# Performance work log

Measured on AMD Instinct MI355X. Metric: run time of the kernel, lower is better.

The kernel has to match this reference:

```python
import jax, jax.numpy as jnp
import numpy as np

EPS = 1e-5

def _layernorm(x, w, b):
    mu = jnp.mean(x, axis=-1, keepdims=True)
    var = jnp.mean(jnp.square(x - mu), axis=-1, keepdims=True)
    return (x - mu) * jax.lax.rsqrt(var + EPS) * w + b

def setup_inputs() -> dict:
    key = jax.random.key(0)
    ks = jax.random.split(key, 6)
    B, Np, Nc, D, P = 2, 512, 512, 128, 128
    p_embed = jax.random.normal(ks[0], (B, Np, D), dtype=jnp.float32)
    c_embed = jax.random.normal(ks[1], (B, Nc, D), dtype=jnp.float32)
    p_mask = jnp.ones((B, Np), dtype=bool)
    c_mask = jnp.ones((B, Nc), dtype=bool)
    ln_p_w = jnp.ones((D,), jnp.float32)
    ln_p_b = jnp.zeros((D,), jnp.float32)
    ln_c_w = jnp.ones((D,), jnp.float32)
    ln_c_b = jnp.zeros((D,), jnp.float32)
    W_out = jax.random.normal(ks[2], (P, D), dtype=jnp.float32) / np.sqrt(D)
    b_out = jax.random.normal(ks[3], (P,), dtype=jnp.float32) * 0.01
    return {"p_embed": p_embed, "c_embed": c_embed, "p_mask": p_mask,
            "c_mask": c_mask, "ln_p_w": ln_p_w, "ln_p_b": ln_p_b,
            "ln_c_w": ln_c_w, "ln_c_b": ln_c_b, "W_out": W_out, "b_out": b_out}

def reference(p_embed, c_embed, p_mask, c_mask, ln_p_w, ln_p_b, ln_c_w, ln_c_b, W_out, b_out):
    # inter_mask[b,i,j] = p_mask[b,i] & c_mask[b,j]
    inter_mask = p_mask[..., :, None] & c_mask[..., None, :]
    p = _layernorm(p_embed, ln_p_w, ln_p_b)  # [B,Np,D]
    c = _layernorm(c_embed, ln_c_w, ln_c_b)  # [B,Nc,D]
    # einsum '...ik,...jk->...ijk' followed by Linear(D->P), fused into one
    # contraction so the [B,Np,Nc,D] intermediate is never materialized:
    # out[b,i,j,h] = sum_k p[b,i,k]*c[b,j,k]*W_out[h,k] + b_out[h]
    inter = jnp.einsum('bik,bjk,hk->bijh', p, c, W_out) + b_out
    inter = inter * inter_mask[..., None].astype(inter.dtype)
    return inter, inter_mask
```

## Files before the change

### kernel.cpp

```cpp
#include <hip/hip_runtime.h>
#include <hip/hip_bf16.h>

#define BATCH 2
#define NP 512
#define NC 512
#define DD 128
#define PP 128

typedef __bf16 bf16_t;
typedef __bf16 bf16x8 __attribute__((ext_vector_type(8)));
typedef float f32x4 __attribute__((ext_vector_type(4)));

__global__ __launch_bounds__(64) void ln_kernel(const float* __restrict__ x,
                                                const float* __restrict__ w,
                                                const float* __restrict__ bsh,
                                                float* __restrict__ y) {
    int row = blockIdx.x;
    int t = threadIdx.x;
    const float* xr = x + (size_t)row * DD;
    float2 v = *(const float2*)&xr[2 * t];
    float s  = v.x + v.y;
    float sq = v.x * v.x + v.y * v.y;
    for (int o = 32; o; o >>= 1) {
        s  += __shfl_xor(s, o);
        sq += __shfl_xor(sq, o);
    }
    float mu  = s * (1.0f / 128.0f);
    float var = sq * (1.0f / 128.0f) - mu * mu;
    float rs  = rsqrtf(var + 1e-5f);
    float2 wv = *(const float2*)&w[2 * t];
    float2 bv = *(const float2*)&bsh[2 * t];
    float* yr = y + (size_t)row * DD;
    float2 o2;
    o2.x = (v.x - mu) * rs * wv.x + bv.x;
    o2.y = (v.y - mu) * rs * wv.y + bv.y;
    *(float2*)&yr[2 * t] = o2;
}

__global__ __launch_bounds__(256) void cvt_kernel(const float* __restrict__ W,
                                                  bf16_t* __restrict__ Wb) {
    int idx = blockIdx.x * 256 + threadIdx.x;
    Wb[idx] = (bf16_t)W[idx];
}

__global__ __launch_bounds__(256) void inter_kernel(
    const float* __restrict__ p_ln, const float* __restrict__ c_ln,
    const bf16_t* __restrict__ Wb, const float* __restrict__ b_out,
    const int* __restrict__ p_mask,
    const int* __restrict__ c_mask,
    float* __restrict__ out) {
    __shared__ bf16_t As[128][136];
    __shared__ bf16_t Ws[128][136];

    int blk = blockIdx.x;
    int jt = blk & 3;
    int i  = (blk >> 2) & 511;
    int b  = blk >> 11;
    int j0 = jt * 128;

    int t = threadIdx.x;
    int kcol = (t & 15) * 8;
    int rgrp = t >> 4;

    const float* prow = p_ln + ((size_t)(b * NP + i)) * DD + kcol;
    float4 p0 = *(const float4*)&prow[0];
    float4 p1 = *(const float4*)&prow[4];

    const float* cbase = c_ln + ((size_t)(b * NC + j0)) * DD;
    #pragma unroll
    for (int pass = 0; pass < 8; ++pass) {
        int row = pass * 16 + rgrp;
        const float* cr = cbase + (size_t)row * DD + kcol;
        float4 c0 = *(const float4*)&cr[0];
        float4 c1 = *(const float4*)&cr[4];
        bf16x8 av;
        av[0] = (bf16_t)(c0.x * p0.x); av[1] = (bf16_t)(c0.y * p0.y);
        av[2] = (bf16_t)(c0.z * p0.z); av[3] = (bf16_t)(c0.w * p0.w);
        av[4] = (bf16_t)(c1.x * p1.x); av[5] = (bf16_t)(c1.y * p1.y);
        av[6] = (bf16_t)(c1.z * p1.z); av[7] = (bf16_t)(c1.w * p1.w);
        *(bf16x8*)&As[row][kcol] = av;
        const bf16_t* wr = Wb + (size_t)row * DD + kcol;
        *(bf16x8*)&Ws[row][kcol] = *(const bf16x8*)wr;
    }
    __syncthreads();

    int lane = t & 63;
    int wave = t >> 6;
    int wm = wave >> 1, wn = wave & 1;
    int m0 = wm * 64, n0 = wn * 64;
    int l16 = lane & 15, q = lane >> 4;

    f32x4 acc[4][4];
    #pragma unroll
    for (int mi = 0; mi < 4; ++mi)
        #pragma unroll
        for (int ni = 0; ni < 4; ++ni)
            acc[mi][ni] = (f32x4){0.f, 0.f, 0.f, 0.f};

    #pragma unroll
    for (int kk = 0; kk < 4; ++kk) {
        int kb = kk * 32 + q * 8;
        bf16x8 a[4], w[4];
        #pragma unroll
        for (int mi = 0; mi < 4; ++mi)
            a[mi] = *(const bf16x8*)&As[m0 + mi * 16 + l16][kb];
        #pragma unroll
        for (int ni = 0; ni < 4; ++ni)
            w[ni] = *(const bf16x8*)&Ws[n0 + ni * 16 + l16][kb];
        #pragma unroll
        for (int mi = 0; mi < 4; ++mi)
            #pragma unroll
            for (int ni = 0; ni < 4; ++ni)
                acc[mi][ni] = __builtin_amdgcn_mfma_f32_16x16x32_bf16(
                    a[mi], w[ni], acc[mi][ni], 0, 0, 0);
    }

    int pm = p_mask[b * NP + i];
    float bias[4];
    #pragma unroll
    for (int ni = 0; ni < 4; ++ni)
        bias[ni] = b_out[n0 + ni * 16 + l16];

    size_t outbase = (((size_t)b * NP + i) * NC) * PP;
    #pragma unroll
    for (int mi = 0; mi < 4; ++mi) {
        #pragma unroll
        for (int reg = 0; reg < 4; ++reg) {
            int j = j0 + m0 + mi * 16 + q * 4 + reg;
            int cm = c_mask[b * NC + j];
            float scale = (pm != 0 && cm != 0) ? 1.0f : 0.0f;
            float* orow = out + outbase + (size_t)j * PP;
            #pragma unroll
            for (int ni = 0; ni < 4; ++ni)
                orow[n0 + ni * 16 + l16] = (acc[mi][ni][reg] + bias[ni]) * scale;
        }
    }

    if (t < 128) {
        int j = j0 + t;
        int cm = c_mask[b * NC + j];
        size_t mbase = (size_t)BATCH * NP * NC * PP;
        out[mbase + ((size_t)b * NP + i) * NC + j] =
            (pm != 0 && cm != 0) ? 1.0f : 0.0f;
    }
}

extern "C" void kernel_launch(void* const* d_in, const int* in_sizes, int n_in,
                              void* d_out, int out_size, void* d_ws, size_t ws_size,
                              hipStream_t stream) {
    const float* p_embed = (const float*)d_in[0];
    const float* c_embed = (const float*)d_in[1];
    const int* p_mask = (const int*)d_in[2];
    const int* c_mask = (const int*)d_in[3];
    const float* ln_p_w = (const float*)d_in[4];
    const float* ln_p_b = (const float*)d_in[5];
    const float* ln_c_w = (const float*)d_in[6];
    const float* ln_c_b = (const float*)d_in[7];
    const float* W_out  = (const float*)d_in[8];
    const float* b_out  = (const float*)d_in[9];
    float* out = (float*)d_out;

    float* p_ln = (float*)d_ws;
    float* c_ln = p_ln + (size_t)BATCH * NP * DD;
    bf16_t* w_bf = (bf16_t*)(c_ln + (size_t)BATCH * NC * DD);

    ln_kernel<<<BATCH * NP, 64, 0, stream>>>(p_embed, ln_p_w, ln_p_b, p_ln);
    ln_kernel<<<BATCH * NC, 64, 0, stream>>>(c_embed, ln_c_w, ln_c_b, c_ln);
    cvt_kernel<<<(PP * DD) / 256, 256, 0, stream>>>(W_out, w_bf);
    inter_kernel<<<BATCH * NP * (NC / 128), 256, 0, stream>>>(
        p_ln, c_ln, w_bf, b_out, p_mask, c_mask, out);
}
```

Measured before the change: 286.1 us.

## Swap MFMA operand roles for vectorized float4 stores and drop W smem tile

Swaps the MFMA operands so W becomes the M side and the p*c product the N side. Each lane's accumulator registers then hold four consecutive output channels, so results go out as 128-bit f32x4 stores instead of scalar stores. W fragments are now read directly from global memory (L2/L1-cached bf16) rather than staged in LDS, which halves shared memory, and a launch bound of 4 blocks per CU is requested. The risk is extra global-load latency for W inside the MFMA loop and register pressure under the tighter launch bound.

Measured after the change: 311.6 us. +8.9%, slower.

```diff
diff --git a/kernel.cpp b/kernel.cpp
--- a/kernel.cpp
+++ b/kernel.cpp
@@ -43,14 +43,13 @@
     Wb[idx] = (bf16_t)W[idx];
 }
 
-__global__ __launch_bounds__(256) void inter_kernel(
+__global__ __launch_bounds__(256, 4) void inter_kernel(
     const float* __restrict__ p_ln, const float* __restrict__ c_ln,
     const bf16_t* __restrict__ Wb, const float* __restrict__ b_out,
     const int* __restrict__ p_mask,
     const int* __restrict__ c_mask,
     float* __restrict__ out) {
-    __shared__ bf16_t As[128][136];
-    __shared__ bf16_t Ws[128][136];
+    __shared__ bf16_t Bs[128][136];
 
     int blk = blockIdx.x;
     int jt = blk & 3;
@@ -78,9 +77,7 @@
         av[2] = (bf16_t)(c0.z * p0.z); av[3] = (bf16_t)(c0.w * p0.w);
         av[4] = (bf16_t)(c1.x * p1.x); av[5] = (bf16_t)(c1.y * p1.y);
         av[6] = (bf16_t)(c1.z * p1.z); av[7] = (bf16_t)(c1.w * p1.w);
-        *(bf16x8*)&As[row][kcol] = av;
-        const bf16_t* wr = Wb + (size_t)row * DD + kcol;
-        *(bf16x8*)&Ws[row][kcol] = *(const bf16x8*)wr;
+        *(bf16x8*)&Bs[row][kcol] = av;
     }
     __syncthreads();
 
@@ -100,39 +97,38 @@
     #pragma unroll
     for (int kk = 0; kk < 4; ++kk) {
         int kb = kk * 32 + q * 8;
-        bf16x8 a[4], w[4];
+        bf16x8 w[4], cp[4];
         #pragma unroll
         for (int mi = 0; mi < 4; ++mi)
-            a[mi] = *(const bf16x8*)&As[m0 + mi * 16 + l16][kb];
+            w[mi] = *(const bf16x8*)&Wb[(size_t)(m0 + mi * 16 + l16) * DD + kb];
         #pragma unroll
         for (int ni = 0; ni < 4; ++ni)
-            w[ni] = *(const bf16x8*)&Ws[n0 + ni * 16 + l16][kb];
+            cp[ni] = *(const bf16x8*)&Bs[n0 + ni * 16 + l16][kb];
         #pragma unroll
         for (int mi = 0; mi < 4; ++mi)
             #pragma unroll
             for (int ni = 0; ni < 4; ++ni)
                 acc[mi][ni] = __builtin_amdgcn_mfma_f32_16x16x32_bf16(
-                    a[mi], w[ni], acc[mi][ni], 0, 0, 0);
+                    w[mi], cp[ni], acc[mi][ni], 0, 0, 0);
     }
 
     int pm = p_mask[b * NP + i];
-    float bias[4];
+    f32x4 biasv[4];
     #pragma unroll
-    for (int ni = 0; ni < 4; ++ni)
-        bias[ni] = b_out[n0 + ni * 16 + l16];
+    for (int mi = 0; mi < 4; ++mi)
+        biasv[mi] = *(const f32x4*)&b_out[m0 + mi * 16 + q * 4];
 
     size_t outbase = (((size_t)b * NP + i) * NC) * PP;
     #pragma unroll
-    for (int mi = 0; mi < 4; ++mi) {
+    for (int ni = 0; ni < 4; ++ni) {
+        int j = j0 + n0 + ni * 16 + l16;
+        int cm = c_mask[b * NC + j];
+        float scale = (pm != 0 && cm != 0) ? 1.0f : 0.0f;
+        float* orow = out + outbase + (size_t)j * PP + m0;
         #pragma unroll
-        for (int reg = 0; reg < 4; ++reg) {
-            int j = j0 + m0 + mi * 16 + q * 4 + reg;
-            int cm = c_mask[b * NC + j];
-            float scale = (pm != 0 && cm != 0) ? 1.0f : 0.0f;
-            float* orow = out + outbase + (size_t)j * PP;
-            #pragma unroll
-            for (int ni = 0; ni < 4; ++ni)
-                orow[n0 + ni * 16 + l16] = (acc[mi][ni][reg] + bias[ni]) * scale;
+        for (int mi = 0; mi < 4; ++mi) {
+            f32x4 v = (acc[mi][ni] + biasv[mi]) * scale;
+            *(f32x4*)&orow[mi * 16 + q * 4] = v;
         }
     }
 
```
